# Optimization experiments

Hardware: AMD Instinct MI355X
Metric: run time of the kernel (lower is better)

## Reference

```python
import jax, jax.numpy as jnp
import numpy as np

B, CIN, COUT, CLEV = 1, 128, 128, 64
H, W = 48, 160            # height//2**scale, width//2**scale (scale=2)
MIN_D, MAX_D = 0.1, 100.0


def conv3x3(x, w, b, mode):
    x = jnp.pad(x, ((0, 0), (0, 0), (1, 1), (1, 1)), mode=mode)
    y = jax.lax.conv_general_dilated(x, w, (1, 1), 'VALID',
                                     dimension_numbers=('NCHW', 'OIHW', 'NCHW'))
    return y + b[None, :, None, None]


def head(x, w1, b1, w2, b2):  # gaussian head: conv -> GELU -> conv, replicate pad
    return conv3x3(jax.nn.gelu(conv3x3(x, w1, b1, 'edge')), w2, b2, 'edge')


def convblock(x, w, b):  # ConvBlock: 3x3 conv (reflect pad) + ELU
    return jax.nn.elu(conv3x3(x, w, b, 'reflect'))


def to_pts(t):  # [B,C,H,W] -> [B,HW,C]
    return t.transpose(0, 2, 3, 1).reshape(t.shape[0], -1, t.shape[1])


def quat_to_rot(q):  # [N,4] (w,x,y,z) -> [N,3,3]
    w, x, y, z = q[:, 0], q[:, 1], q[:, 2], q[:, 3]
    return jnp.stack([1 - 2 * (y * y + z * z), 2 * (x * y - w * z), 2 * (x * z + w * y),
                      2 * (x * y + w * z), 1 - 2 * (x * x + z * z), 2 * (y * z - w * x),
                      2 * (x * z - w * y), 2 * (y * z + w * x), 1 - 2 * (x * x + y * y)],
                     axis=-1).reshape(-1, 3, 3)


def rasterize_one(pos, rot, scl, opa, feat, K):
    # depth-sort gaussians front-to-back
    order = jnp.argsort(pos[:, 2])
    pos, rot, scl, opa, feat = pos[order], rot[order], scl[order], opa[order], feat[order]
    x, y, z = pos[:, 0], pos[:, 1], pos[:, 2]
    fx, fy, cx, cy = K[0, 0], K[1, 1], K[0, 2], K[1, 2]
    u, v = fx * x / z + cx, fy * y / z + cy
    # 3D covariance Sigma = R S S^T R^T, projected with perspective Jacobian J
    M = quat_to_rot(rot) * scl[:, None, :]
    Sig = jnp.einsum('nij,nkj->nik', M, M)
    zer = jnp.zeros_like(z)
    J = jnp.stack([fx / z, zer, -fx * x / z ** 2,
                   zer, fy / z, -fy * y / z ** 2], axis=-1).reshape(-1, 2, 3)
    cov = jnp.einsum('nij,njk,nlk->nil', J, Sig, J)
    a = cov[:, 0, 0] + 0.3  # low-pass blur as in 3DGS
    bq = cov[:, 0, 1]
    c = cov[:, 1, 1] + 0.3
    det = a * c - bq * bq
    A, Bc, C = c / det, -bq / det, a / det  # conic (inverse 2D covariance)
    gy, gx = jnp.meshgrid(jnp.arange(H, dtype=pos.dtype),
                          jnp.arange(W, dtype=pos.dtype), indexing='ij')
    dx = gx.reshape(-1)[:, None] - u[None, :]  # [P,N]
    dy = gy.reshape(-1)[:, None] - v[None, :]
    power = -0.5 * (A[None] * dx * dx + C[None] * dy * dy) - Bc[None] * dx * dy
    alpha = jnp.where(power <= 0.,
                      jnp.clip(opa[None, :, 0] * jnp.exp(jnp.minimum(power, 0.)), 0., 0.99),
                      0.)
    l1m = jnp.log1p(-alpha)
    logT = jnp.cumsum(l1m, axis=1) - l1m  # exclusive transmittance along sorted axis
    wgt = alpha * jnp.exp(logT)           # [P,N]
    return (wgt @ feat).T.reshape(-1, H, W)  # [C,H,W]


def forward(init_feature, disp_init, inv_K, K,
            rot_w1, rot_b1, rot_w2, rot_b2,
            scl_w1, scl_b1, scl_w2, scl_b2,
            opa_w1, opa_b1, opa_w2, opa_b2,
            fl_w1, fl_b1, fl_w2, fl_b2, fr_w, fr_b):
    bs = init_feature.shape[0]
    # disp_to_depth
    scaled = 1. / MAX_D + (1. / MIN_D - 1. / MAX_D) * disp_init
    depth = jnp.clip(1. / scaled, MIN_D, MAX_D)
    # backproject depth to a point cloud
    gy, gx = jnp.meshgrid(jnp.arange(H, dtype=depth.dtype),
                          jnp.arange(W, dtype=depth.dtype), indexing='ij')
    pix = jnp.stack([gx.ravel(), gy.ravel(), jnp.ones(H * W, depth.dtype)], 0)  # [3,HW]
    cam = jnp.einsum('bij,jn->bin', inv_K[:, :3, :3], pix) * depth.reshape(bs, 1, -1)
    position = cam.transpose(0, 2, 1)  # [B,N,3]
    rot = head(init_feature, rot_w1, rot_b1, rot_w2, rot_b2)
    rot = rot / jnp.maximum(jnp.linalg.norm(rot, axis=1, keepdims=True), 1e-12)
    rotation = to_pts(rot)  # [B,N,4]
    scale = to_pts(jnp.abs(head(init_feature, scl_w1, scl_b1, scl_w2, scl_b2)))
    opacity = to_pts(jax.nn.sigmoid(head(init_feature, opa_w1, opa_b1, opa_w2, opa_b2)))
    gs_feat = to_pts(convblock(convblock(init_feature, fl_w1, fl_b1), fl_w2, fl_b2))
    lev = jax.vmap(rasterize_one)(position, rotation, scale, opacity, gs_feat, K)
    return convblock(lev, fr_w, fr_b)


def setup_inputs() -> dict:
    key = jax.random.key(0)
    ks = jax.random.split(key, 16)
    p = lambda i, shape: jax.random.normal(ks[i], shape, jnp.float32) * 0.05
    Kmat = np.array([[0.58 * W, 0, 0.5 * W, 0],
                     [0, 1.92 * H, 0.5 * H, 0],
                     [0, 0, 1, 0],
                     [0, 0, 0, 1]], dtype=np.float32)
    inv_K = np.linalg.inv(Kmat)
    return {
        'init_feature': jax.random.normal(ks[0], (B, CIN, H, W), jnp.float32),
        'disp_init': jax.random.uniform(ks[1], (B, 1, H, W), jnp.float32, 0.01, 0.99),
        'inv_K': jnp.tile(jnp.asarray(inv_K)[None], (B, 1, 1)),
        'K': jnp.tile(jnp.asarray(Kmat)[None], (B, 1, 1)),
        'rot_w1': p(2, (8, CIN, 3, 3)), 'rot_b1': jnp.zeros(8),
        'rot_w2': p(3, (4, 8, 3, 3)), 'rot_b2': jnp.zeros(4),
        'scl_w1': p(4, (6, CIN, 3, 3)), 'scl_b1': jnp.zeros(6),
        'scl_w2': p(5, (3, 6, 3, 3)), 'scl_b2': jnp.zeros(3),
        'opa_w1': p(6, (2, CIN, 3, 3)), 'opa_b1': jnp.zeros(2),
        'opa_w2': p(7, (1, 2, 3, 3)), 'opa_b2': jnp.zeros(1),
        'fl_w1': p(8, (CIN, CIN, 3, 3)), 'fl_b1': jnp.zeros(CIN),
        'fl_w2': p(9, (CLEV, CIN, 3, 3)), 'fl_b2': jnp.zeros(CLEV),
        'fr_w': p(10, (COUT, CLEV, 3, 3)), 'fr_b': jnp.zeros(COUT),
    }


def reference(init_feature, disp_init, inv_K, K, rot_w1, rot_b1, rot_w2, rot_b2,
              scl_w1, scl_b1, scl_w2, scl_b2, opa_w1, opa_b1, opa_w2, opa_b2,
              fl_w1, fl_b1, fl_w2, fl_b2, fr_w, fr_b):
    return forward(init_feature, disp_init, inv_K, K, rot_w1, rot_b1, rot_w2, rot_b2,
                   scl_w1, scl_b1, scl_w2, scl_b2, opa_w1, opa_b1, opa_w2, opa_b2,
                   fl_w1, fl_b1, fl_w2, fl_b2, fr_w, fr_b)
```

## Files before the change

kernel.cpp:

```cpp
#include <hip/hip_runtime.h>
#include <hip/hip_bf16.h>
#include <math.h>

#define Hh 48
#define Ww 160
#define NP 7680

using bf16 = __hip_bfloat16;
typedef __attribute__((ext_vector_type(8))) short v8s;
typedef __attribute__((ext_vector_type(4))) float v4f;

__device__ __forceinline__ float bfdec(unsigned short u) {
  return __uint_as_float(((unsigned)u) << 16);
}
__device__ __forceinline__ unsigned short bfenc(float x) {
  bf16 b = __float2bfloat16(x);
  return *(unsigned short*)&b;
}
__device__ __forceinline__ v8s ldv8(const unsigned short* p) {
  return *(const v8s*)p;
}
__device__ __forceinline__ float ldany(const void* p, size_t i, int isbf) {
  return isbf ? bfdec(((const unsigned short*)p)[i]) : ((const float*)p)[i];
}

__device__ __forceinline__ int mapidx(int i, int n, int mode) {
  if (mode == 0) return i < 0 ? 0 : (i >= n ? n - 1 : i);
  return i < 0 ? -i : (i >= n ? 2 * n - 2 - i : i);
}

__device__ __forceinline__ float eluf(float v) { return v > 0.f ? v : expm1f(v); }
__device__ __forceinline__ float geluf(float v) {
  float c = v + 0.044715f * v * v * v;
  return 0.5f * v * (1.f + tanhf(0.7978845608028654f * c));
}

__device__ __forceinline__ float zkey(float d, float lin) {
  float scaled = fmaf(9.99f, d, 0.01f);
  float depth = fminf(fmaxf(1.f / scaled, 0.1f), 100.f);
  return lin * depth;
}

__device__ __forceinline__ int sniff_local(const unsigned short* w, int* cnt) {
  int c = 0;
  for (int i = threadIdx.x; i < 2048; i += 256) {
    float a = fabsf(bfdec(w[i]));
    if (a > 1e-3f && a < 0.5f) c++;
  }
  cnt[threadIdx.x] = c;
  __syncthreads();
  for (int s = 128; s > 0; s >>= 1) {
    if (threadIdx.x < s) cnt[threadIdx.x] += cnt[threadIdx.x + s];
    __syncthreads();
  }
  int f = (cnt[0] > 1536) ? 1 : 0;
  __syncthreads();
  return f;
}

__global__ __launch_bounds__(256) void prep_all_k(int* __restrict__ flag,
    const void* __restrict__ xsrc, unsigned short* __restrict__ xb,
    const void* disp, const void* invK, const void* K, const void* rw2,
    const void* rb2, const void* sw2, const void* sb2, const void* ow2, const void* ob2,
    const void* rb1, const void* sb1, const void* ob1, const void* fb1, const void* fb2,
    const void* frb, const void* rot_w1, const void* scl_w1, const void* opa_w1,
    const void* fl_w1, const void* fl_w2, const void* fr_w,
    float* __restrict__ dispf, float* __restrict__ smallf, float* __restrict__ biasf,
    unsigned short* __restrict__ a_h1, unsigned short* __restrict__ a_fl1,
    unsigned short* __restrict__ a_fl2, unsigned short* __restrict__ a_fr) {
  __shared__ float tile[32][33];
  __shared__ int cnt[256];
  const int f = sniff_local((const unsigned short*)fl_w1, cnt);
  if (blockIdx.x == 0 && threadIdx.x == 0) flag[0] = f;
  if (blockIdx.x < 960) {
    const int bx = blockIdx.x;
    const int pb = (bx % 240) * 32, cb = (bx / 240) * 32;
#pragma unroll
    for (int pass = 0; pass < 4; pass++) {
      int ci = (threadIdx.x >> 5) + pass * 8, pl = threadIdx.x & 31;
      tile[ci][pl] = ldany(xsrc, (size_t)(cb + ci) * NP + pb + pl, f);
    }
    __syncthreads();
#pragma unroll
    for (int pass = 0; pass < 4; pass++) {
      int pl = (threadIdx.x >> 5) + pass * 8, ci = threadIdx.x & 31;
      xb[(size_t)(pb + pl) * 128 + cb + ci] = bfenc(tile[ci][pl]);
    }
    return;
  }
  int i = (blockIdx.x - 960) * 256 + threadIdx.x;
  if (i < 7680) { dispf[i] = ldany(disp, i, f); return; }
  i -= 7680;
  if (i < 508) {
    const void* src; int off;
    if (i < 16)       { src = invK; off = i; }
    else if (i < 32)  { src = K;    off = i - 16; }
    else if (i < 320) { src = rw2;  off = i - 32; }
    else if (i < 324) { src = rb2;  off = i - 320; }
    else if (i < 486) { src = sw2;  off = i - 324; }
    else if (i < 489) { src = sb2;  off = i - 486; }
    else if (i < 507) { src = ow2;  off = i - 489; }
    else              { src = ob2;  off = i - 507; }
    smallf[i] = ldany(src, off, f); return;
  }
  i -= 508;
  if (i < 336) {
    if (i < 8) biasf[i] = ldany(rb1, i, f);
    else if (i < 14) biasf[i] = ldany(sb1, i - 8, f);
    else if (i < 16) biasf[i] = ldany(ob1, i - 14, f);
    else if (i < 144) biasf[i] = ldany(fb1, i - 16, f);
    else if (i < 208) biasf[i] = ldany(fb2, i - 144, f);
    else biasf[i] = ldany(frb, i - 208, f);
    return;
  }
  i -= 336;
  if (i < 73728) {
    int co = i / 1152, rem = i - co * 1152;
    int t = rem >> 7, ci = rem & 127;
    float v = 0.f;
    if (co < 8) v = ldany(rot_w1, (size_t)co * 1152 + ci * 9 + t, f);
    else if (co < 14) v = ldany(scl_w1, (size_t)(co - 8) * 1152 + ci * 9 + t, f);
    else if (co < 16) v = ldany(opa_w1, (size_t)(co - 14) * 1152 + ci * 9 + t, f);
    a_h1[i] = bfenc(v); return;
  }
  i -= 73728;
  if (i < 147456) {
    int co = i / 1152, rem = i - co * 1152;
    int t = rem >> 7, ci = rem & 127;
    a_fl1[i] = bfenc(ldany(fl_w1, (size_t)co * 1152 + ci * 9 + t, f)); return;
  }
  i -= 147456;
  if (i < 73728) {
    int co = i / 1152, rem = i - co * 1152;
    int t = rem >> 7, ci = rem & 127;
    a_fl2[i] = bfenc(ldany(fl_w2, (size_t)co * 1152 + ci * 9 + t, f)); return;
  }
  i -= 73728;
  if (i < 73728) {
    int co = i / 576, rem = i - co * 576;
    int t = rem >> 6, ci = rem & 63;
    a_fr[i] = bfenc(ldany(fr_w, (size_t)co * 576 + ci * 9 + t, f));
    return;
  }
}

template<int OM, int PM, int ACT, int KP>
__global__ __launch_bounds__(256) void gemm_conv32_k(const unsigned short* __restrict__ A,
    const unsigned short* __restrict__ X, const float* __restrict__ bias,
    void* __restrict__ out, const int* __restrict__ flag, int K) {
  __shared__ __align__(16) unsigned char smem[16512];
  v8s (*As4)[64][5] = (v8s (*)[64][5])smem;
  v8s (*Bs4)[32][5] = (v8s (*)[32][5])(smem + 10240);
  int (*off9s)[9]   = (int (*)[9])(smem + 15360);
  const int tid = threadIdx.x;
  const int pxB = blockIdx.x * 32;
  const int coB = blockIdx.y * 64;
  if (tid < 32) {
    int p = pxB + tid;
    int h = p / Ww, w = p - h * Ww;
#pragma unroll
    for (int r = 0; r < 3; r++) {
      int hh = mapidx(h + r - 1, Hh, PM);
#pragma unroll
      for (int s = 0; s < 3; s++)
        off9s[tid][r * 3 + s] = hh * Ww + mapidx(w + s - 1, Ww, PM);
    }
  }
  const int lane = tid & 63, wv = tid >> 6;
  const int m16 = lane & 15, quad = lane >> 4;
  const int srow = tid >> 2, sg = tid & 3;
  v4f acc[2];
#pragma unroll
  for (int b = 0; b < 2; b++) acc[b] = (v4f){0.f, 0.f, 0.f, 0.f};
  __syncthreads();
  const int nIter = K >> 5;
  auto loadA = [&](int it) {
    return ldv8(&A[(size_t)(coB + srow) * K + (it << 5) + sg * 8]);
  };
  auto loadB = [&](int it) {
    const int k0 = it << 5;
    if (KP == 128) {
      int kk = k0 + sg * 8;
      return ldv8(&X[(size_t)off9s[srow][kk >> 7] * 128 + (kk & 127)]);
    } else {
      int kk = k0 + sg * 8;
      return ldv8(&X[(size_t)off9s[srow][kk >> 6] * 64 + (kk & 63)]);
    }
  };
  {
    v8s av0 = loadA(0);
    As4[0][srow][sg] = av0;
    if (srow < 32) {
      v8s bv0 = loadB(0);
      Bs4[0][srow][sg] = bv0;
    }
  }
  __syncthreads();
  int cur = 0;
  v8s avn, bvn;
  for (int it = 0; it < nIter; it++) {
    if (it + 1 < nIter) {
      avn = loadA(it + 1);
      if (srow < 32) bvn = loadB(it + 1);
    }
    v8s af = As4[cur][wv * 16 + m16][quad];
    v8s bfr[2];
#pragma unroll
    for (int b = 0; b < 2; b++) bfr[b] = Bs4[cur][b * 16 + m16][quad];
#pragma unroll
    for (int b = 0; b < 2; b++)
      acc[b] = __builtin_amdgcn_mfma_f32_16x16x32_bf16(af, bfr[b], acc[b], 0, 0, 0);
    if (it + 1 < nIter) {
      As4[cur ^ 1][srow][sg] = avn;
      if (srow < 32) Bs4[cur ^ 1][srow][sg] = bvn;
    }
    __syncthreads();
    cur ^= 1;
  }
  const int obf = (OM == 2) ? *flag : (OM == 1);
#pragma unroll
  for (int b = 0; b < 2; b++) {
#pragma unroll
    for (int r = 0; r < 4; r++) {
      int co = coB + wv * 16 + quad * 4 + r;
      int px = pxB + b * 16 + m16;
      float bv = bias[co];
      float v = acc[b][r] + bv;
      v = (ACT == 2) ? geluf(v) : eluf(v);
      size_t oi = (size_t)co * NP + px;
      if (obf) ((unsigned short*)out)[oi] = bfenc(v);
      else ((float*)out)[oi] = v;
    }
  }
}

__global__ __launch_bounds__(256) void conv_fused1_k(
    const unsigned short* __restrict__ a_fl1, const unsigned short* __restrict__ a_h1,
    const unsigned short* __restrict__ X, const float* __restrict__ biasf,
    const float* __restrict__ dispf, const float* __restrict__ smallf,
    unsigned short* __restrict__ t1b, float* __restrict__ h1,
    int* __restrict__ ord) {
  __shared__ __align__(16) unsigned char smem[31872];
  const int tid = threadIdx.x;
  const int zy = blockIdx.y;
  if (zy == 3) {
    if (blockIdx.x >= 120) return;
    float* zsrt = (float*)smem;
    int (*part)[4] = (int (*)[4])(smem + 30848);
    const float M20 = smallf[8], M21 = smallf[9], M22 = smallf[10];
    for (int i2 = tid; i2 < NP; i2 += 256) {
      int gy = i2 / Ww, gx = i2 - gy * Ww;
      int s = i2 / 1920, pos = i2 - s * 1920;
      zsrt[s * 1928 + pos] = zkey(dispf[i2],
                                  fmaf(M20, (float)gx, fmaf(M21, (float)gy, M22)));
    }
    __syncthreads();
    const int g = tid >> 2, seg = tid & 3;
    const int i = blockIdx.x * 64 + g;
    const int si = i / 1920, pi = i - si * 1920;
    const float zi = zsrt[si * 1928 + pi];
    const float4* zv = (const float4*)(zsrt + seg * 1928);
    int c = 0;
    for (int t = 0; t < 480; t++) {
      float4 z4 = zv[t];
      int jb = seg * 1920 + t * 4;
      c += (z4.x < zi || (z4.x == zi && jb + 0 < i)) ? 1 : 0;
      c += (z4.y < zi || (z4.y == zi && jb + 1 < i)) ? 1 : 0;
      c += (z4.z < zi || (z4.z == zi && jb + 2 < i)) ? 1 : 0;
      c += (z4.w < zi || (z4.w == zi && jb + 3 < i)) ? 1 : 0;
    }
    part[g][seg] = c;
    __syncthreads();
    if (seg == 0) {
      ord[part[g][0] + part[g][1] + part[g][2] + part[g][3]] = i;
    }
    return;
  }
  v8s (*As4)[64][5] = (v8s (*)[64][5])smem;
  v8s (*Bs4)[32][5] = (v8s (*)[32][5])(smem + 10240);
  int (*off9s)[9]   = (int (*)[9])(smem + 15360);
  const bool ishead = (zy == 2);
  const int pm = ishead ? 0 : 1;
  const int pxB = blockIdx.x * 32;
  const int coB = ishead ? 0 : zy * 64;
  const unsigned short* A = ishead ? a_h1 : a_fl1;
  if (tid < 32) {
    int p = pxB + tid;
    int h = p / Ww, w = p - h * Ww;
#pragma unroll
    for (int r = 0; r < 3; r++) {
      int hh = mapidx(h + r - 1, Hh, pm);
#pragma unroll
      for (int s = 0; s < 3; s++)
        off9s[tid][r * 3 + s] = hh * Ww + mapidx(w + s - 1, Ww, pm);
    }
  }
  const int lane = tid & 63, wv = tid >> 6;
  const int m16 = lane & 15, quad = lane >> 4;
  const int srow = tid >> 2, sg = tid & 3;
  v4f acc[2];
#pragma unroll
  for (int b = 0; b < 2; b++) acc[b] = (v4f){0.f, 0.f, 0.f, 0.f};
  __syncthreads();
  auto loadA = [&](int it) {
    return ldv8(&A[(size_t)(coB + srow) * 1152 + (it << 5) + sg * 8]);
  };
  auto loadB = [&](int it) {
    int kk = (it << 5) + sg * 8;
    return ldv8(&X[(size_t)off9s[srow][kk >> 7] * 128 + (kk & 127)]);
  };
  {
    v8s av0 = loadA(0);
    As4[0][srow][sg] = av0;
    if (srow < 32) {
      v8s bv0 = loadB(0);
      Bs4[0][srow][sg] = bv0;
    }
  }
  __syncthreads();
  int cur = 0;
  v8s avn, bvn;
  for (int it = 0; it < 36; it++) {
    if (it + 1 < 36) {
      avn = loadA(it + 1);
      if (srow < 32) bvn = loadB(it + 1);
    }
    v8s af = As4[cur][wv * 16 + m16][quad];
    v8s bfr[2];
#pragma unroll
    for (int b = 0; b < 2; b++) bfr[b] = Bs4[cur][b * 16 + m16][quad];
#pragma unroll
    for (int b = 0; b < 2; b++)
      acc[b] = __builtin_amdgcn_mfma_f32_16x16x32_bf16(af, bfr[b], acc[b], 0, 0, 0);
    if (it + 1 < 36) {
      As4[cur ^ 1][srow][sg] = avn;
      if (srow < 32) Bs4[cur ^ 1][srow][sg] = bvn;
    }
    __syncthreads();
    cur ^= 1;
  }
  if (ishead) {
#pragma unroll
    for (int b = 0; b < 2; b++) {
#pragma unroll
      for (int r = 0; r < 4; r++) {
        int co = coB + wv * 16 + quad * 4 + r;
        int px = pxB + b * 16 + m16;
        if (co < 16) h1[(size_t)co * NP + px] = geluf(acc[b][r] + biasf[co]);
      }
    }
  } else {
    const int cb = coB + wv * 16 + quad * 4;
#pragma unroll
    for (int b = 0; b < 2; b++) {
      int px = pxB + b * 16 + m16;
      ushort4 o;
      o.x = bfenc(eluf(acc[b][0] + biasf[16 + cb + 0]));
      o.y = bfenc(eluf(acc[b][1] + biasf[16 + cb + 1]));
      o.z = bfenc(eluf(acc[b][2] + biasf[16 + cb + 2]));
      o.w = bfenc(eluf(acc[b][3] + biasf[16 + cb + 3]));
      *(ushort4*)&t1b[(size_t)px * 128 + cb] = o;
    }
  }
}

__global__ __launch_bounds__(256) void fl2_head2_k(
    const unsigned short* __restrict__ a_fl2, const unsigned short* __restrict__ t1b,
    const float* __restrict__ biasf, unsigned short* __restrict__ t2eb,
    const float* __restrict__ h1, const float* __restrict__ smallf,
    const float* __restrict__ dispf, float* __restrict__ params) {
  __shared__ __align__(16) unsigned char smem[16512];
  const int tid = threadIdx.x;
  if (blockIdx.x < 240) {
    v8s (*As4)[64][5] = (v8s (*)[64][5])smem;
    v8s (*Bs4)[32][5] = (v8s (*)[32][5])(smem + 10240);
    int (*off9s)[9]   = (int (*)[9])(smem + 15360);
    const int pxB = blockIdx.x * 32;
    if (tid < 32) {
      int p = pxB + tid;
      int h = p / Ww, w = p - h * Ww;
#pragma unroll
      for (int r = 0; r < 3; r++) {
        int hh = mapidx(h + r - 1, Hh, 1);
#pragma unroll
        for (int s = 0; s < 3; s++)
          off9s[tid][r * 3 + s] = hh * Ww + mapidx(w + s - 1, Ww, 1);
      }
    }
    const int lane = tid & 63, wv = tid >> 6;
    const int m16 = lane & 15, quad = lane >> 4;
    const int srow = tid >> 2, sg = tid & 3;
    v4f acc[2];
#pragma unroll
    for (int b = 0; b < 2; b++) acc[b] = (v4f){0.f, 0.f, 0.f, 0.f};
    __syncthreads();
    auto loadA = [&](int it) {
      return ldv8(&a_fl2[(size_t)srow * 1152 + (it << 5) + sg * 8]);
    };
    auto loadB = [&](int it) {
      int kk = (it << 5) + sg * 8;
      return ldv8(&t1b[(size_t)off9s[srow][kk >> 7] * 128 + (kk & 127)]);
    };
    {
      v8s av0 = loadA(0);
      As4[0][srow][sg] = av0;
      if (srow < 32) {
        v8s bv0 = loadB(0);
        Bs4[0][srow][sg] = bv0;
      }
    }
    __syncthreads();
    int cur = 0;
    v8s avn, bvn;
    for (int it = 0; it < 36; it++) {
      if (it + 1 < 36) {
        avn = loadA(it + 1);
        if (srow < 32) bvn = loadB(it + 1);
      }
      v8s af = As4[cur][wv * 16 + m16][quad];
      v8s bfr[2];
#pragma unroll
      for (int b = 0; b < 2; b++) bfr[b] = Bs4[cur][b * 16 + m16][quad];
#pragma unroll
      for (int b = 0; b < 2; b++)
        acc[b] = __builtin_amdgcn_mfma_f32_16x16x32_bf16(af, bfr[b], acc[b], 0, 0, 0);
      if (it + 1 < 36) {
        As4[cur ^ 1][srow][sg] = avn;
        if (srow < 32) Bs4[cur ^ 1][srow][sg] = bvn;
      }
      __syncthreads();
      cur ^= 1;
    }
#pragma unroll
    for (int b = 0; b < 2; b++) {
#pragma unroll
      for (int r = 0; r < 4; r++) {
        int co = wv * 16 + quad * 4 + r;
        int px = pxB + b * 16 + m16;
        t2eb[(size_t)co * NP + px] = bfenc(eluf(acc[b][r] + biasf[144 + co]));
      }
    }
    return;
  }
  const float* invK = smallf;
  const float* Km   = smallf + 16;
  const float* rw2  = smallf + 32;
  const float* rb2  = smallf + 320;
  const float* sw2  = smallf + 324;
  const float* sb2  = smallf + 486;
  const float* ow2  = smallf + 489;
  const float* ob2  = smallf + 507;
  int p = (blockIdx.x - 240) * 256 + tid;
  if (p >= NP) return;
  int hh = p / Ww, ww = p - hh * Ww;
  float racc[4], sacc[3], oacc;
#pragma unroll
  for (int i = 0; i < 4; i++) racc[i] = rb2[i];
#pragma unroll
  for (int i = 0; i < 3; i++) sacc[i] = sb2[i];
  oacc = ob2[0];
  for (int ci = 0; ci < 16; ci++) {
    float t9[9];
#pragma unroll
    for (int r = 0; r < 3; r++) {
      int rr = mapidx(hh + r - 1, Hh, 0);
#pragma unroll
      for (int s = 0; s < 3; s++) {
        int cc = mapidx(ww + s - 1, Ww, 0);
        t9[r * 3 + s] = h1[(size_t)ci * NP + rr * Ww + cc];
      }
    }
    if (ci < 8) {
      for (int co = 0; co < 4; co++)
#pragma unroll
        for (int k = 0; k < 9; k++)
          racc[co] = fmaf(t9[k], rw2[(co * 8 + ci) * 9 + k], racc[co]);
    } else if (ci < 14) {
      int c2 = ci - 8;
      for (int co = 0; co < 3; co++)
#pragma unroll
        for (int k = 0; k < 9; k++)
          sacc[co] = fmaf(t9[k], sw2[(co * 6 + c2) * 9 + k], sacc[co]);
    } else {
      int c2 = ci - 14;
#pragma unroll
      for (int k = 0; k < 9; k++)
        oacc = fmaf(t9[k], ow2[c2 * 9 + k], oacc);
    }
  }
  float nq = sqrtf(racc[0]*racc[0] + racc[1]*racc[1] + racc[2]*racc[2] + racc[3]*racc[3]);
  nq = fmaxf(nq, 1e-12f);
  float qw = racc[0] / nq, qx = racc[1] / nq, qy = racc[2] / nq, qz = racc[3] / nq;
  float s0 = fabsf(sacc[0]), s1 = fabsf(sacc[1]), s2 = fabsf(sacc[2]);
  float opa = 1.f / (1.f + __expf(-oacc));
  float d = dispf[p];
  float scaled = 0.01f + 9.99f * d;
  float depth = fminf(fmaxf(1.f / scaled, 0.1f), 100.f);
  float M00 = invK[0], M01 = invK[1], M02 = invK[2];
  float M10 = invK[4], M11 = invK[5], M12 = invK[6];
  float M20 = invK[8], M21 = invK[9], M22 = invK[10];
  float gxf = (float)ww, gyf = (float)hh;
  float X = (M00 * gxf + M01 * gyf + M02) * depth;
  float Y = (M10 * gxf + M11 * gyf + M12) * depth;
  float Z = (M20 * gxf + M21 * gyf + M22) * depth;
  float fxk = Km[0], fyk = Km[5];
  float cxk = Km[2], cyk = Km[6];
  float u = fxk * X / Z + cxk;
  float v = fyk * Y / Z + cyk;
  float R00 = 1.f - 2.f*(qy*qy + qz*qz), R01 = 2.f*(qx*qy - qw*qz), R02 = 2.f*(qx*qz + qw*qy);
  float R10 = 2.f*(qx*qy + qw*qz), R11 = 1.f - 2.f*(qx*qx + qz*qz), R12 = 2.f*(qy*qz - qw*qx);
  float R20 = 2.f*(qx*qz - qw*qy), R21 = 2.f*(qy*qz + qw*qx), R22 = 1.f - 2.f*(qx*qx + qy*qy);
  float M0a = R00*s0, M0b = R01*s1, M0c = R02*s2;
  float M1a = R10*s0, M1b = R11*s1, M1c = R12*s2;
  float M2a = R20*s0, M2b = R21*s1, M2c = R22*s2;
  float S00 = M0a*M0a + M0b*M0b + M0c*M0c;
  float S01 = M0a*M1a + M0b*M1b + M0c*M1c;
  float S02 = M0a*M2a + M0b*M2b + M0c*M2c;
  float S11 = M1a*M1a + M1b*M1b + M1c*M1c;
  float S12 = M1a*M2a + M1b*M2b + M1c*M2c;
  float S22 = M2a*M2a + M2b*M2b + M2c*M2c;
  float iz = 1.f / Z;
  float j00 = fxk * iz, j02 = -fxk * X * iz * iz;
  float j11 = fyk * iz, j12 = -fyk * Y * iz * iz;
  float c00 = j00*j00*S00 + 2.f*j00*j02*S02 + j02*j02*S22 + 0.3f;
  float c01 = j00*j11*S01 + j00*j12*S02 + j02*j11*S12 + j02*j12*S22;
  float c11 = j11*j11*S11 + 2.f*j11*j12*S12 + j12*j12*S22 + 0.3f;
  float det = c00 * c11 - c01 * c01;
  float idet = 1.f / det;
  float* pr = params + (size_t)p * 8;
  pr[0] = u; pr[1] = v; pr[2] = c11 * idet; pr[3] = -c01 * idet;
  pr[4] = c00 * idet; pr[5] = opa; pr[6] = Z; pr[7] = 0.f;
}

__global__ __launch_bounds__(64) void raster_seq_k(const int* __restrict__ ord,
    const float* __restrict__ params, const unsigned short* __restrict__ t2eb,
    unsigned short* __restrict__ levb) {
  __shared__ unsigned int Wl[64][17];
  __shared__ int ords[32];
  const int lane = threadIdx.x;
  const int m16 = lane & 15, quad = lane >> 4;
  const int pxB = blockIdx.x * 64;
  const int mypx = pxB + lane;
  const float px = (float)(mypx % Ww), py = (float)(mypx / Ww);
  float T = 1.f;
  v4f acc[4][4];
#pragma unroll
  for (int a = 0; a < 4; a++)
#pragma unroll
    for (int b = 0; b < 4; b++) acc[a][b] = (v4f){0.f, 0.f, 0.f, 0.f};
  for (int sub = 0; sub < NP / 32; sub++) {
    const int g0 = sub * 32;
    if (lane < 32) ords[lane] = ord[g0 + lane];
    __syncthreads();
    int myord[8];
#pragma unroll
    for (int j = 0; j < 8; j++) myord[j] = ords[quad * 8 + j];
    float al[32];
#pragma unroll
    for (int j = 0; j < 32; j++) {
      const float* pp = params + ((size_t)ords[j] << 3);
      float4 pa = *(const float4*)pp;
      float4 pb = *(const float4*)(pp + 4);
      float dx = px - pa.x, dy = py - pa.y;
      float power = -0.5f * (pa.z * dx * dx + pb.x * dy * dy) - pa.w * dx * dy;
      al[j] = fminf(pb.y * __expf(power), 0.99f);
    }
#pragma unroll
    for (int jj = 0; jj < 16; jj++) {
      float w0 = al[2 * jj] * T;     T *= 1.f - al[2 * jj];
      float w1 = al[2 * jj + 1] * T; T *= 1.f - al[2 * jj + 1];
      Wl[lane][jj] = (unsigned)bfenc(w0) | ((unsigned)bfenc(w1) << 16);
    }
    v8s af[4], bfr[4];
#pragma unroll
    for (int a = 0; a < 4; a++) {
      unsigned d0 = Wl[a * 16 + m16][quad * 4 + 0];
      unsigned d1 = Wl[a * 16 + m16][quad * 4 + 1];
      unsigned d2 = Wl[a * 16 + m16][quad * 4 + 2];
      unsigned d3 = Wl[a * 16 + m16][quad * 4 + 3];
      v8s t;
      t[0] = (short)(d0 & 0xffff); t[1] = (short)(d0 >> 16);
      t[2] = (short)(d1 & 0xffff); t[3] = (short)(d1 >> 16);
      t[4] = (short)(d2 & 0xffff); t[5] = (short)(d2 >> 16);
      t[6] = (short)(d3 & 0xffff); t[7] = (short)(d3 >> 16);
      af[a] = t;
    }
#pragma unroll
    for (int b = 0; b < 4; b++) {
      const unsigned short* fp = &t2eb[(size_t)(b * 16 + m16) * NP];
      v8s t;
#pragma unroll
      for (int j = 0; j < 8; j++) t[j] = (short)fp[myord[j]];
      bfr[b] = t;
    }
#pragma unroll
    for (int a = 0; a < 4; a++)
#pragma unroll
      for (int b = 0; b < 4; b++)
        acc[a][b] = __builtin_amdgcn_mfma_f32_16x16x32_bf16(af[a], bfr[b], acc[a][b], 0, 0, 0);
    if (__all(T < 1e-7f)) break;
    __syncthreads();
  }
#pragma unroll
  for (int a = 0; a < 4; a++) {
#pragma unroll
    for (int b = 0; b < 4; b++) {
#pragma unroll
      for (int r = 0; r < 4; r++) {
        levb[(size_t)(pxB + a * 16 + quad * 4 + r) * 64 + b * 16 + m16] =
            bfenc(acc[a][b][r]);
      }
    }
  }
}

extern "C" void kernel_launch(void* const* d_in, const int* in_sizes, int n_in,
                              void* d_out, int out_size, void* d_ws, size_t ws_size,
                              hipStream_t stream) {
  (void)in_sizes; (void)n_in; (void)out_size; (void)ws_size;
  const void* init_feature = d_in[0];
  const void* disp   = d_in[1];
  const void* invK   = d_in[2];
  const void* Km     = d_in[3];
  const void* rot_w1 = d_in[4];
  const void* rot_b1 = d_in[5];
  const void* rot_w2 = d_in[6];
  const void* rot_b2 = d_in[7];
  const void* scl_w1 = d_in[8];
  const void* scl_b1 = d_in[9];
  const void* scl_w2 = d_in[10];
  const void* scl_b2 = d_in[11];
  const void* opa_w1 = d_in[12];
  const void* opa_b1 = d_in[13];
  const void* opa_w2 = d_in[14];
  const void* opa_b2 = d_in[15];
  const void* fl_w1  = d_in[16];
  const void* fl_b1  = d_in[17];
  const void* fl_w2  = d_in[18];
  const void* fl_b2  = d_in[19];
  const void* fr_w   = d_in[20];
  const void* fr_b   = d_in[21];

  float* wsf = (float*)d_ws;
  int*   flag    = (int*)wsf;
  float* smallf  = wsf + 16;
  float* dispf   = wsf + 528;
  float* biasf   = wsf + 8208;
  unsigned short* a_h1  = (unsigned short*)(wsf + 8720);
  unsigned short* a_fl1 = (unsigned short*)(wsf + 45584);
  unsigned short* a_fl2 = (unsigned short*)(wsf + 119312);
  unsigned short* a_fr  = (unsigned short*)(wsf + 156176);
  unsigned short* xb    = (unsigned short*)(wsf + 193040);
  unsigned short* t1b   = (unsigned short*)(wsf + 684560);
  unsigned short* t2eb  = (unsigned short*)(wsf + 1176080);
  float* h1      = wsf + 1667600;
  float* params  = wsf + 1790480;
  unsigned short* levb = (unsigned short*)(wsf + 2896400);
  int*   ord     = (int*)(wsf + 3157520);

  prep_all_k<<<2434, 256, 0, stream>>>(flag, init_feature, xb,
      disp, invK, Km, rot_w2, rot_b2, scl_w2, scl_b2, opa_w2, opa_b2,
      rot_b1, scl_b1, opa_b1, fl_b1, fl_b2, fr_b,
      rot_w1, scl_w1, opa_w1, fl_w1, fl_w2, fr_w,
      dispf, smallf, biasf, a_h1, a_fl1, a_fl2, a_fr);

  conv_fused1_k<<<dim3(240, 4), 256, 0, stream>>>(a_fl1, a_h1, xb, biasf,
                                                  dispf, smallf, t1b, h1, ord);
  fl2_head2_k<<<270, 256, 0, stream>>>(a_fl2, t1b, biasf, t2eb, h1, smallf,
                                       dispf, params);
  raster_seq_k<<<120, 64, 0, stream>>>(ord, params, t2eb, levb);
  gemm_conv32_k<2, 1, 1, 64><<<dim3(240, 2), 256, 0, stream>>>(
      a_fr, levb, biasf + 208, d_out, flag, 576);
}
```

Baseline: 203.4 us.

## Stage conv input halo in shared memory once instead of im2col double-buffering

```diff
diff --git a/kernel.cpp b/kernel.cpp
--- a/kernel.cpp
+++ b/kernel.cpp
@@ -56,6 +56,38 @@
   int f = (cnt[0] > 1536) ? 1 : 0;
   __syncthreads();
   return f;
+}
+
+template<int NCH, int PADR, int K, int PM>
+__device__ __forceinline__ void halo_conv(const unsigned short* __restrict__ A,
+    const unsigned short* __restrict__ X, unsigned short* hx,
+    int pxB, int coB, int tid, v4f acc[2]) {
+  const int row0 = pxB / Ww, c0 = pxB - row0 * Ww;
+  constexpr int CH8 = NCH / 8;
+  for (int idx = tid; idx < 102 * CH8; idx += 256) {
+    int e = idx / CH8, ch = (idx - e * CH8) * 8;
+    int r = e / 34, j = e - r * 34;
+    int gr = mapidx(row0 + r - 1, Hh, PM);
+    int gc = mapidx(c0 + j - 1, Ww, PM);
+    *(v8s*)&hx[(size_t)e * PADR + ch] = ldv8(&X[((size_t)gr * Ww + gc) * NCH + ch]);
+  }
+  __syncthreads();
+  const int lane = tid & 63, wv = tid >> 6;
+  const int m16 = lane & 15, quad = lane >> 4;
+  acc[0] = (v4f){0.f, 0.f, 0.f, 0.f};
+  acc[1] = (v4f){0.f, 0.f, 0.f, 0.f};
+  const unsigned short* arow = &A[(size_t)(coB + wv * 16 + m16) * K + quad * 8];
+#pragma unroll
+  for (int it = 0; it < K / 32; it++) {
+    const int kk = it * 32;
+    const int t = kk / NCH, within = kk - t * NCH;
+    const int r = t / 3, s = t - r * 3;
+    v8s af = ldv8(&arow[kk]);
+    v8s b0 = ldv8(&hx[(size_t)(r * 34 + m16 + s) * PADR + within + quad * 8]);
+    v8s b1 = ldv8(&hx[(size_t)(r * 34 + 16 + m16 + s) * PADR + within + quad * 8]);
+    acc[0] = __builtin_amdgcn_mfma_f32_16x16x32_bf16(af, b0, acc[0], 0, 0, 0);
+    acc[1] = __builtin_amdgcn_mfma_f32_16x16x32_bf16(af, b1, acc[1], 0, 0, 0);
+  }
 }
 
 __global__ __launch_bounds__(256) void prep_all_k(int* __restrict__ flag,
@@ -144,89 +176,25 @@
   }
 }
 
-template<int OM, int PM, int ACT, int KP>
 __global__ __launch_bounds__(256) void gemm_conv32_k(const unsigned short* __restrict__ A,
     const unsigned short* __restrict__ X, const float* __restrict__ bias,
-    void* __restrict__ out, const int* __restrict__ flag, int K) {
-  __shared__ __align__(16) unsigned char smem[16512];
-  v8s (*As4)[64][5] = (v8s (*)[64][5])smem;
-  v8s (*Bs4)[32][5] = (v8s (*)[32][5])(smem + 10240);
-  int (*off9s)[9]   = (int (*)[9])(smem + 15360);
+    void* __restrict__ out, const int* __restrict__ flag) {
+  __shared__ __align__(16) unsigned short hx[102 * 72];
   const int tid = threadIdx.x;
   const int pxB = blockIdx.x * 32;
   const int coB = blockIdx.y * 64;
-  if (tid < 32) {
-    int p = pxB + tid;
-    int h = p / Ww, w = p - h * Ww;
-#pragma unroll
-    for (int r = 0; r < 3; r++) {
-      int hh = mapidx(h + r - 1, Hh, PM);
-#pragma unroll
-      for (int s = 0; s < 3; s++)
-        off9s[tid][r * 3 + s] = hh * Ww + mapidx(w + s - 1, Ww, PM);
-    }
-  }
+  v4f acc[2];
+  halo_conv<64, 72, 576, 1>(A, X, hx, pxB, coB, tid, acc);
   const int lane = tid & 63, wv = tid >> 6;
   const int m16 = lane & 15, quad = lane >> 4;
-  const int srow = tid >> 2, sg = tid & 3;
-  v4f acc[2];
-#pragma unroll
-  for (int b = 0; b < 2; b++) acc[b] = (v4f){0.f, 0.f, 0.f, 0.f};
-  __syncthreads();
-  const int nIter = K >> 5;
-  auto loadA = [&](int it) {
-    return ldv8(&A[(size_t)(coB + srow) * K + (it << 5) + sg * 8]);
-  };
-  auto loadB = [&](int it) {
-    const int k0 = it << 5;
-    if (KP == 128) {
-      int kk = k0 + sg * 8;
-      return ldv8(&X[(size_t)off9s[srow][kk >> 7] * 128 + (kk & 127)]);
-    } else {
-      int kk = k0 + sg * 8;
-      return ldv8(&X[(size_t)off9s[srow][kk >> 6] * 64 + (kk & 63)]);
-    }
-  };
-  {
-    v8s av0 = loadA(0);
-    As4[0][srow][sg] = av0;
-    if (srow < 32) {
-      v8s bv0 = loadB(0);
-      Bs4[0][srow][sg] = bv0;
-    }
-  }
-  __syncthreads();
-  int cur = 0;
-  v8s avn, bvn;
-  for (int it = 0; it < nIter; it++) {
-    if (it + 1 < nIter) {
-      avn = loadA(it + 1);
-      if (srow < 32) bvn = loadB(it + 1);
-    }
-    v8s af = As4[cur][wv * 16 + m16][quad];
-    v8s bfr[2];
-#pragma unroll
-    for (int b = 0; b < 2; b++) bfr[b] = Bs4[cur][b * 16 + m16][quad];
-#pragma unroll
-    for (int b = 0; b < 2; b++)
-      acc[b] = __builtin_amdgcn_mfma_f32_16x16x32_bf16(af, bfr[b], acc[b], 0, 0, 0);
-    if (it + 1 < nIter) {
-      As4[cur ^ 1][srow][sg] = avn;
-      if (srow < 32) Bs4[cur ^ 1][srow][sg] = bvn;
-    }
-    __syncthreads();
-    cur ^= 1;
-  }
-  const int obf = (OM == 2) ? *flag : (OM == 1);
+  const int obf = *flag;
 #pragma unroll
   for (int b = 0; b < 2; b++) {
 #pragma unroll
     for (int r = 0; r < 4; r++) {
       int co = coB + wv * 16 + quad * 4 + r;
       int px = pxB + b * 16 + m16;
-      float bv = bias[co];
-      float v = acc[b][r] + bv;
-      v = (ACT == 2) ? geluf(v) : eluf(v);
+      float v = eluf(acc[b][r] + bias[co]);
       size_t oi = (size_t)co * NP + px;
       if (obf) ((unsigned short*)out)[oi] = bfenc(v);
       else ((float*)out)[oi] = v;
@@ -276,69 +244,16 @@
     }
     return;
   }
-  v8s (*As4)[64][5] = (v8s (*)[64][5])smem;
-  v8s (*Bs4)[32][5] = (v8s (*)[32][5])(smem + 10240);
-  int (*off9s)[9]   = (int (*)[9])(smem + 15360);
+  unsigned short* hx = (unsigned short*)smem;
   const bool ishead = (zy == 2);
-  const int pm = ishead ? 0 : 1;
   const int pxB = blockIdx.x * 32;
   const int coB = ishead ? 0 : zy * 64;
   const unsigned short* A = ishead ? a_h1 : a_fl1;
-  if (tid < 32) {
-    int p = pxB + tid;
-    int h = p / Ww, w = p - h * Ww;
-#pragma unroll
-    for (int r = 0; r < 3; r++) {
-      int hh = mapidx(h + r - 1, Hh, pm);
-#pragma unroll
-      for (int s = 0; s < 3; s++)
-        off9s[tid][r * 3 + s] = hh * Ww + mapidx(w + s - 1, Ww, pm);
-    }
-  }
+  v4f acc[2];
+  if (ishead) halo_conv<128, 136, 1152, 0>(A, X, hx, pxB, coB, tid, acc);
+  else        halo_conv<128, 136, 1152, 1>(A, X, hx, pxB, coB, tid, acc);
   const int lane = tid & 63, wv = tid >> 6;
   const int m16 = lane & 15, quad = lane >> 4;
-  const int srow = tid >> 2, sg = tid & 3;
-  v4f acc[2];
-#pragma unroll
-  for (int b = 0; b < 2; b++) acc[b] = (v4f){0.f, 0.f, 0.f, 0.f};
-  __syncthreads();
-  auto loadA = [&](int it) {
-    return ldv8(&A[(size_t)(coB + srow) * 1152 + (it << 5) + sg * 8]);
-  };
-  auto loadB = [&](int it) {
-    int kk = (it << 5) + sg * 8;
-    return ldv8(&X[(size_t)off9s[srow][kk >> 7] * 128 + (kk & 127)]);
-  };
-  {
-    v8s av0 = loadA(0);
-    As4[0][srow][sg] = av0;
-    if (srow < 32) {
-      v8s bv0 = loadB(0);
-      Bs4[0][srow][sg] = bv0;
-    }
-  }
-  __syncthreads();
-  int cur = 0;
-  v8s avn, bvn;
-  for (int it = 0; it < 36; it++) {
-    if (it + 1 < 36) {
-      avn = loadA(it + 1);
-      if (srow < 32) bvn = loadB(it + 1);
-    }
-    v8s af = As4[cur][wv * 16 + m16][quad];
-    v8s bfr[2];
-#pragma unroll
-    for (int b = 0; b < 2; b++) bfr[b] = Bs4[cur][b * 16 + m16][quad];
-#pragma unroll
-    for (int b = 0; b < 2; b++)
-      acc[b] = __builtin_amdgcn_mfma_f32_16x16x32_bf16(af, bfr[b], acc[b], 0, 0, 0);
-    if (it + 1 < 36) {
-      As4[cur ^ 1][srow][sg] = avn;
-      if (srow < 32) Bs4[cur ^ 1][srow][sg] = bvn;
-    }
-    __syncthreads();
-    cur ^= 1;
-  }
   if (ishead) {
 #pragma unroll
     for (int b = 0; b < 2; b++) {
@@ -369,68 +284,14 @@
     const float* __restrict__ biasf, unsigned short* __restrict__ t2eb,
     const float* __restrict__ h1, const float* __restrict__ smallf,
     const float* __restrict__ dispf, float* __restrict__ params) {
-  __shared__ __align__(16) unsigned char smem[16512];
+  __shared__ __align__(16) unsigned short hx[102 * 136];
   const int tid = threadIdx.x;
   if (blockIdx.x < 240) {
-    v8s (*As4)[64][5] = (v8s (*)[64][5])smem;
-    v8s (*Bs4)[32][5] = (v8s (*)[32][5])(smem + 10240);
-    int (*off9s)[9]   = (int (*)[9])(smem + 15360);
     const int pxB = blockIdx.x * 32;
-    if (tid < 32) {
-      int p = pxB + tid;
-      int h = p / Ww, w = p - h * Ww;
-#pragma unroll
-      for (int r = 0; r < 3; r++) {
-        int hh = mapidx(h + r - 1, Hh, 1);
-#pragma unroll
-        for (int s = 0; s < 3; s++)
-          off9s[tid][r * 3 + s] = hh * Ww + mapidx(w + s - 1, Ww, 1);
-      }
-    }
+    v4f acc[2];
+    halo_conv<128, 136, 1152, 1>(a_fl2, t1b, hx, pxB, 0, tid, acc);
     const int lane = tid & 63, wv = tid >> 6;
     const int m16 = lane & 15, quad = lane >> 4;
-    const int srow = tid >> 2, sg = tid & 3;
-    v4f acc[2];
-#pragma unroll
-    for (int b = 0; b < 2; b++) acc[b] = (v4f){0.f, 0.f, 0.f, 0.f};
-    __syncthreads();
-    auto loadA = [&](int it) {
-      return ldv8(&a_fl2[(size_t)srow * 1152 + (it << 5) + sg * 8]);
-    };
-    auto loadB = [&](int it) {
-      int kk = (it << 5) + sg * 8;
-      return ldv8(&t1b[(size_t)off9s[srow][kk >> 7] * 128 + (kk & 127)]);
-    };
-    {
-      v8s av0 = loadA(0);
-      As4[0][srow][sg] = av0;
-      if (srow < 32) {
-        v8s bv0 = loadB(0);
-        Bs4[0][srow][sg] = bv0;
-      }
-    }
-    __syncthreads();
-    int cur = 0;
-    v8s avn, bvn;
-    for (int it = 0; it < 36; it++) {
-      if (it + 1 < 36) {
-        avn = loadA(it + 1);
-        if (srow < 32) bvn = loadB(it + 1);
-      }
-      v8s af = As4[cur][wv * 16 + m16][quad];
-      v8s bfr[2];
-#pragma unroll
-      for (int b = 0; b < 2; b++) bfr[b] = Bs4[cur][b * 16 + m16][quad];
-#pragma unroll
-      for (int b = 0; b < 2; b++)
-        acc[b] = __builtin_amdgcn_mfma_f32_16x16x32_bf16(af, bfr[b], acc[b], 0, 0, 0);
-      if (it + 1 < 36) {
-        As4[cur ^ 1][srow][sg] = avn;
-        if (srow < 32) Bs4[cur ^ 1][srow][sg] = bvn;
-      }
-      __syncthreads();
-      cur ^= 1;
-    }
 #pragma unroll
     for (int b = 0; b < 2; b++) {
 #pragma unroll
@@ -669,6 +530,6 @@
   fl2_head2_k<<<270, 256, 0, stream>>>(a_fl2, t1b, biasf, t2eb, h1, smallf,
                                        dispf, params);
   raster_seq_k<<<120, 64, 0, stream>>>(ord, params, t2eb, levb);
-  gemm_conv32_k<2, 1, 1, 64><<<dim3(240, 2), 256, 0, stream>>>(
-      a_fr, levb, biasf + 208, d_out, flag, 576);
-}
+  gemm_conv32_k<<<dim3(240, 2), 256, 0, stream>>>(
+      a_fr, levb, biasf + 208, d_out, flag);
+}
```

Measured after the change: 198.9 us. 2.2% less time.
